# Performance work log

Hardware: AMD Instinct MI355X
Metric: run time of the kernel (lower is better)

Reference implementation:

```python
import jax, jax.numpy as jnp
import numpy as np

N = 384        # n_res
C = 128        # c_pair
H = 4          # num_head
DH = C // H    # qkv_dim = 32
LN_EPS = 1e-5
NEG_INF = -1e9


def setup_inputs() -> dict:
    key = jax.random.key(0)
    ks = jax.random.split(key, 8)
    s = 0.02
    return {
        "pair": jax.random.normal(ks[0], (N, N, C), dtype=jnp.float32),
        "mask": jax.random.randint(ks[1], (N, N), 0, 2, dtype=jnp.int32),
        "ln_w": jnp.ones((C,), dtype=jnp.float32),
        "ln_b": jnp.zeros((C,), dtype=jnp.float32),
        "w_bias": jax.random.normal(ks[2], (C, H), dtype=jnp.float32) * s,
        "wq": jax.random.normal(ks[3], (C, C), dtype=jnp.float32) * s,
        "wk": jax.random.normal(ks[4], (C, C), dtype=jnp.float32) * s,
        "wv": jax.random.normal(ks[5], (C, C), dtype=jnp.float32) * s,
        "wg": jax.random.normal(ks[6], (C, C), dtype=jnp.float32) * s,
        "wo": jax.random.normal(ks[7], (C, C), dtype=jnp.float32) * s,
    }


def reference(pair, mask, ln_w, ln_b, w_bias, wq, wk, wv, wg, wo):
    # LayerNorm over c_pair (biased variance, as torch)
    mu = pair.mean(-1, keepdims=True)
    var = jnp.mean(jnp.square(pair - mu), axis=-1, keepdims=True)
    x = (pair - mu) * jax.lax.rsqrt(var + LN_EPS) * ln_w + ln_b  # [N,N,C]

    # per-head pair bias: [H, N, N] (query axis q, key axis k)
    bias = jnp.einsum('qkc,ch->hqk', x, w_bias)

    # QKV + gating projections (no bias)
    q = jnp.einsum('bkc,cd->bkd', x, wq).reshape(N, N, H, DH)
    k = jnp.einsum('bkc,cd->bkd', x, wk).reshape(N, N, H, DH)
    v = jnp.einsum('bkc,cd->bkd', x, wv).reshape(N, N, H, DH)

    scale = 1.0 / np.sqrt(DH).astype(np.float32)
    logits = jnp.einsum('bqhd,bkhd->bhqk', q, k) * scale + bias[None]  # [N,H,N,N]
    # mask[b, k]: disallow attending to masked keys in row b
    logits = jnp.where(mask[:, None, None, :] > 0, logits, NEG_INF)
    probs = jax.nn.softmax(logits, axis=-1)

    o = jnp.einsum('bhqk,bkhd->bqhd', probs, v).reshape(N, N, C)
    gate = jax.nn.sigmoid(jnp.einsum('bqc,cd->bqd', x, wg))
    out = jnp.einsum('bqc,cd->bqd', o * gate, wo)  # [N,N,C]
    return out
```

## Files before the change

kernel.cpp:

```cpp
#include <hip/hip_runtime.h>
#include <hip/hip_bf16.h>
#include <stdint.h>

#define NRES 384
#define CPAIR 128
#define NHEAD 4
#define DHEAD 32
#define MROWS (NRES * NRES)
#define QK_SCALE 0.17677669529663687f
#define LOG2E 1.4426950408889634f
#define QK_L2E (0.17677669529663687f * 1.4426950408889634f)

typedef unsigned short u16;
typedef short bf16x8 __attribute__((ext_vector_type(8)));
typedef float f32x4 __attribute__((ext_vector_type(4)));

__device__ __forceinline__ u16 f2bf(float f) {
  union { float f; uint32_t u; } c; c.f = f;
  uint32_t u = c.u + 0x7fff + ((c.u >> 16) & 1);
  return (u16)(u >> 16);
}
__device__ __forceinline__ float bf2f(u16 h) {
  union { uint32_t u; float f; } c; c.u = ((uint32_t)h) << 16; return c.f;
}
__device__ __forceinline__ float fast_exp2(float x) {
#if __has_builtin(__builtin_amdgcn_exp2f)
  return __builtin_amdgcn_exp2f(x);
#else
  return exp2f(x);
#endif
}
__device__ __forceinline__ uint32_t cvt_pk_bf16(float lo, float hi) {
  uint32_t r;
  asm("v_cvt_pk_bf16_f32 %0, %1, %2" : "=v"(r) : "v"(lo), "v"(hi));
  return r;
}

__global__ void prep_kernel(const float* __restrict__ wq, const float* __restrict__ wk,
                            const float* __restrict__ wv, const float* __restrict__ wg,
                            const float* __restrict__ wb, const float* __restrict__ wo,
                            u16* __restrict__ wcat, u16* __restrict__ wot) {
  int tid = blockIdx.x * blockDim.x + threadIdx.x;
  int stride = gridDim.x * blockDim.x;
  for (int i = tid; i < 576 * 128; i += stride) {
    int n = i >> 7, kk = i & 127;
    float val;
    if (n < 128)      val = wq[kk * 128 + n] * QK_L2E;
    else if (n < 256) val = wk[kk * 128 + (n - 128)];
    else if (n < 384) val = wv[kk * 128 + (n - 256)];
    else if (n < 512) val = wg[kk * 128 + (n - 384)];
    else if (n < 516) val = wb[kk * 4 + (n - 512)] * LOG2E;
    else              val = 0.f;
    wcat[i] = f2bf(val);
  }
  for (int i = tid; i < 128 * 128; i += stride) {
    int n = i >> 7, kk = i & 127;
    wot[i] = f2bf(wo[kk * 128 + n]);
  }
}

__global__ __launch_bounds__(256) void proj_kernel(
    const float* __restrict__ pair, const float* __restrict__ lnw,
    const float* __restrict__ lnb, const u16* __restrict__ wcat,
    u16* __restrict__ q, u16* __restrict__ k, u16* __restrict__ v,
    u16* __restrict__ g, float* __restrict__ biasL) {
  __shared__ __align__(16) u16 xs[64 * 136];
  __shared__ __align__(16) u16 wsm[64 * 136];
  const int m0 = blockIdx.x * 64;
  const int tid = threadIdx.x;
  {
    const int row = tid >> 2, q4 = tid & 3;
    const float* pr = pair + (size_t)(m0 + row) * CPAIR + q4 * 32;
    float4 vals[8];
    float s1 = 0.f, s2 = 0.f;
#pragma unroll
    for (int i = 0; i < 8; ++i) {
      vals[i] = ((const float4*)pr)[i];
      s1 += (vals[i].x + vals[i].y) + (vals[i].z + vals[i].w);
      s2 += vals[i].x * vals[i].x + vals[i].y * vals[i].y +
            vals[i].z * vals[i].z + vals[i].w * vals[i].w;
    }
    s1 += __shfl_xor(s1, 1); s1 += __shfl_xor(s1, 2);
    s2 += __shfl_xor(s2, 1); s2 += __shfl_xor(s2, 2);
    const float mu = s1 * (1.f / 128.f);
    const float rs = rsqrtf(s2 * (1.f / 128.f) - mu * mu + 1e-5f);
    const float* wr = lnw + q4 * 32;
    const float* br = lnb + q4 * 32;
    uint32_t packed[16];
#pragma unroll
    for (int i = 0; i < 8; ++i) {
      float4 w4 = ((const float4*)wr)[i];
      float4 b4 = ((const float4*)br)[i];
      float y0 = (vals[i].x - mu) * rs * w4.x + b4.x;
      float y1 = (vals[i].y - mu) * rs * w4.y + b4.y;
      float y2 = (vals[i].z - mu) * rs * w4.z + b4.z;
      float y3 = (vals[i].w - mu) * rs * w4.w + b4.w;
      packed[i * 2]     = (uint32_t)f2bf(y0) | ((uint32_t)f2bf(y1) << 16);
      packed[i * 2 + 1] = (uint32_t)f2bf(y2) | ((uint32_t)f2bf(y3) << 16);
    }
#pragma unroll
    for (int i = 0; i < 4; ++i)
      *(uint4*)&xs[row * 136 + q4 * 32 + i * 8] = *(uint4*)&packed[i * 4];
  }
  const int w = tid >> 6, lane = tid & 63, lm = lane & 15, quad = lane >> 4;
  for (int nc = 0; nc < 9; ++nc) {
    __syncthreads();
#pragma unroll
    for (int i = 0; i < 4; ++i) {
      int c = tid + i * 256;
      int row = c >> 4, col8 = (c & 15) * 8;
      *(uint4*)&wsm[row * 136 + col8] =
          *(const uint4*)&wcat[(size_t)(nc * 64 + row) * CPAIR + col8];
    }
    __syncthreads();
    f32x4 acc[4] = {{0, 0, 0, 0}, {0, 0, 0, 0}, {0, 0, 0, 0}, {0, 0, 0, 0}};
#pragma unroll
    for (int ks = 0; ks < 4; ++ks) {
      bf16x8 a = *(const bf16x8*)&xs[(w * 16 + lm) * 136 + ks * 32 + quad * 8];
#pragma unroll
      for (int nt = 0; nt < 4; ++nt) {
        bf16x8 bb = *(const bf16x8*)&wsm[(nt * 16 + lm) * 136 + ks * 32 + quad * 8];
        acc[nt] = __builtin_amdgcn_mfma_f32_16x16x32_bf16(a, bb, acc[nt], 0, 0, 0);
      }
    }
#pragma unroll
    for (int nt = 0; nt < 4; ++nt) {
      int n = nc * 64 + nt * 16 + lm;
#pragma unroll
      for (int r = 0; r < 4; ++r) {
        size_t m = (size_t)(m0 + w * 16 + quad * 4 + r);
        float val = acc[nt][r];
        if (n < 128)      q[m * CPAIR + n] = f2bf(val);
        else if (n < 256) k[m * CPAIR + (n - 128)] = f2bf(val);
        else if (n < 384) v[m * CPAIR + (n - 256)] = f2bf(val);
        else if (n < 512) g[m * CPAIR + (n - 384)] = f2bf(1.f / (1.f + __expf(-val)));
        else if (n < 516) {
          int h = n - 512;
          int q_idx = (int)(m / NRES), k_idx = (int)(m % NRES);
          int qt = q_idx >> 6, l6 = q_idx & 63;
          int ww = l6 >> 4, lmq = l6 & 15;
          int t = k_idx >> 4, qk = (k_idx >> 2) & 3, rk = k_idx & 3;
          size_t idx = ((size_t)((h * 6 + qt) * 24 + t) * 256 +
                        (ww * 64 + qk * 16 + lmq)) * 4 + rk;
          biasL[idx] = val;
        }
      }
    }
  }
}

__global__ __launch_bounds__(512, 4) void attn_kernel(
    const u16* __restrict__ q, const u16* __restrict__ k, const u16* __restrict__ v,
    const u16* __restrict__ g, const float* __restrict__ biasL, const int* __restrict__ mask,
    u16* __restrict__ og) {
  __shared__ __align__(16) u16 Ks[NRES * 40];
  __shared__ __align__(16) u16 Vt[DHEAD * 392];
  __shared__ __align__(16) float msk[NRES];

  const int b = blockIdx.x, h = blockIdx.y;
  const int tid = threadIdx.x;
  const int w = tid >> 6, lane = tid & 63, lm = lane & 15, quad = lane >> 4;
  const int wv = w & 3, hi = w >> 2;

  const u16* kb = k + (size_t)(b * NRES) * CPAIR + h * DHEAD;
  const u16* vb = v + (size_t)(b * NRES) * CPAIR + h * DHEAD;
  for (int i = tid; i < NRES * 4; i += 512) {
    int kk = i >> 2, c8 = (i & 3) * 8;
    *(uint4*)&Ks[kk * 40 + c8] = *(const uint4*)&kb[(size_t)kk * CPAIR + c8];
  }
  for (int i = tid; i < NRES * 4; i += 512) {
    int d8 = i & 3, kk = i >> 2;
    bf16x8 val = *(const bf16x8*)&vb[(size_t)kk * CPAIR + d8 * 8];
    int G = (kk >> 5) * 4 + ((kk >> 2) & 3);
    int e = (kk & 3) + 4 * ((kk >> 4) & 1);
    int col = (((G ^ d8) << 3) | e);
#pragma unroll
    for (int j = 0; j < 8; ++j) Vt[(d8 * 8 + j) * 392 + col] = (u16)val[j];
  }
  for (int i = tid; i < NRES; i += 512)
    msk[i] = (mask[b * NRES + i] > 0) ? 1.f : 0.f;
  __syncthreads();

  const int f0 = lm >> 3, f1 = (lm + 16) >> 3;

  for (int it = 0; it < 3; ++it) {
    const int qt = hi * 3 + it;
    const int q0 = qt * 64;
    bf16x8 af = *(const bf16x8*)&q[(size_t)(b * NRES + q0 + wv * 16 + lm) * CPAIR +
                                   h * DHEAD + quad * 8];
    const float* bptr = biasL + ((size_t)(h * 6 + qt) * 24) * 1024 + (wv * 64 + lane) * 4;
    float rsum = 0.f;
    f32x4 o0 = {0, 0, 0, 0}, o1 = {0, 0, 0, 0};
#pragma unroll
    for (int c = 0; c < 12; ++c) {
      f32x4 s[2];
#pragma unroll
      for (int tl = 0; tl < 2; ++tl) {
        int t = c * 2 + tl;
        bf16x8 kf = *(const bf16x8*)&Ks[(t * 16 + lm) * 40 + quad * 8];
        f32x4 bv = *(const f32x4*)(bptr + t * 1024);
        s[tl] = __builtin_amdgcn_mfma_f32_16x16x32_bf16(kf, af, bv, 0, 0, 0);
      }
      uint32_t pw[4];
#pragma unroll
      for (int tl = 0; tl < 2; ++tl) {
        int t = c * 2 + tl;
        f32x4 m4 = *(const f32x4*)&msk[t * 16 + quad * 4];
        float p0 = fast_exp2(s[tl][0]) * m4[0];
        float p1 = fast_exp2(s[tl][1]) * m4[1];
        float p2 = fast_exp2(s[tl][2]) * m4[2];
        float p3 = fast_exp2(s[tl][3]) * m4[3];
        rsum += (p0 + p1) + (p2 + p3);
        pw[tl * 2]     = cvt_pk_bf16(p0, p1);
        pw[tl * 2 + 1] = cvt_pk_bf16(p2, p3);
      }
      union { uint32_t u[4]; bf16x8 v8; } pf;
      pf.u[0] = pw[0]; pf.u[1] = pw[1]; pf.u[2] = pw[2]; pf.u[3] = pw[3];
      int B0i = c * 4 + quad;
      bf16x8 vt0 = *(const bf16x8*)&Vt[lm * 392 + ((B0i ^ f0) << 3)];
      bf16x8 vt1 = *(const bf16x8*)&Vt[(lm + 16) * 392 + ((B0i ^ f1) << 3)];
      o0 = __builtin_amdgcn_mfma_f32_16x16x32_bf16(pf.v8, vt0, o0, 0, 0, 0);
      o1 = __builtin_amdgcn_mfma_f32_16x16x32_bf16(pf.v8, vt1, o1, 0, 0, 0);
    }
    rsum += __shfl_xor(rsum, 16);
    rsum += __shfl_xor(rsum, 32);
#pragma unroll
    for (int r = 0; r < 4; ++r) {
      float rall = __shfl(rsum, quad * 4 + r);
      float rinv = 1.f / rall;
      size_t mrow = (size_t)(b * NRES + q0 + wv * 16 + quad * 4 + r);
      int c0 = h * DHEAD + lm, c1 = h * DHEAD + 16 + lm;
      float g0 = bf2f(g[mrow * CPAIR + c0]);
      float g1 = bf2f(g[mrow * CPAIR + c1]);
      og[mrow * CPAIR + c0] = f2bf(o0[r] * rinv * g0);
      og[mrow * CPAIR + c1] = f2bf(o1[r] * rinv * g1);
    }
  }
}

__global__ __launch_bounds__(256) void outproj_kernel(const u16* __restrict__ og,
                                                      const u16* __restrict__ wot,
                                                      float* __restrict__ out) {
  __shared__ __align__(16) u16 xs[64 * 136];
  __shared__ __align__(16) u16 wsm[64 * 136];
  const int m0 = blockIdx.x * 64;
  const int tid = threadIdx.x;
#pragma unroll
  for (int i = 0; i < 4; ++i) {
    int c = tid + i * 256;
    int row = c >> 4, col8 = (c & 15) * 8;
    *(uint4*)&xs[row * 136 + col8] = *(const uint4*)&og[(size_t)(m0 + row) * CPAIR + col8];
  }
  const int w = tid >> 6, lane = tid & 63, lm = lane & 15, quad = lane >> 4;
  for (int nc = 0; nc < 2; ++nc) {
    __syncthreads();
#pragma unroll
    for (int i = 0; i < 4; ++i) {
      int c = tid + i * 256;
      int row = c >> 4, col8 = (c & 15) * 8;
      *(uint4*)&wsm[row * 136 + col8] =
          *(const uint4*)&wot[(size_t)(nc * 64 + row) * CPAIR + col8];
    }
    __syncthreads();
    f32x4 acc[4] = {{0, 0, 0, 0}, {0, 0, 0, 0}, {0, 0, 0, 0}, {0, 0, 0, 0}};
#pragma unroll
    for (int ks = 0; ks < 4; ++ks) {
      bf16x8 a = *(const bf16x8*)&xs[(w * 16 + lm) * 136 + ks * 32 + quad * 8];
#pragma unroll
      for (int nt = 0; nt < 4; ++nt) {
        bf16x8 bb = *(const bf16x8*)&wsm[(nt * 16 + lm) * 136 + ks * 32 + quad * 8];
        acc[nt] = __builtin_amdgcn_mfma_f32_16x16x32_bf16(a, bb, acc[nt], 0, 0, 0);
      }
    }
#pragma unroll
    for (int nt = 0; nt < 4; ++nt) {
      int n = nc * 64 + nt * 16 + lm;
#pragma unroll
      for (int r = 0; r < 4; ++r) {
        size_t m = (size_t)(m0 + w * 16 + quad * 4 + r);
        out[m * CPAIR + n] = acc[nt][r];
      }
    }
  }
}

extern "C" void kernel_launch(void* const* d_in, const int* in_sizes, int n_in,
                              void* d_out, int out_size, void* d_ws, size_t ws_size,
                              hipStream_t stream) {
  const float* pair = (const float*)d_in[0];
  const int* mask = (const int*)d_in[1];
  const float* ln_w = (const float*)d_in[2];
  const float* ln_b = (const float*)d_in[3];
  const float* w_bias = (const float*)d_in[4];
  const float* wq = (const float*)d_in[5];
  const float* wk = (const float*)d_in[6];
  const float* wv = (const float*)d_in[7];
  const float* wg = (const float*)d_in[8];
  const float* wo = (const float*)d_in[9];
  float* out = (float*)d_out;

  u16* qb = (u16*)d_out;
  u16* gb = qb + (size_t)MROWS * CPAIR;

  char* ws = (char*)d_ws;
  const size_t SZ = (size_t)MROWS * CPAIR * 2;
  u16* og = (u16*)(ws);
  u16* kb = (u16*)(ws + SZ);
  u16* vb = (u16*)(ws + 2 * SZ);
  float* biasL = (float*)(ws + 3 * SZ);
  u16* wcat = (u16*)(ws + 3 * SZ + (size_t)NHEAD * MROWS * 4);
  u16* wot = wcat + 576 * 128;

  hipLaunchKernelGGL(prep_kernel, dim3(64), dim3(256), 0, stream,
                     wq, wk, wv, wg, w_bias, wo, wcat, wot);
  hipLaunchKernelGGL(proj_kernel, dim3(MROWS / 64), dim3(256), 0, stream,
                     pair, ln_w, ln_b, wcat, qb, kb, vb, gb, biasL);
  hipLaunchKernelGGL(attn_kernel, dim3(NRES, NHEAD), dim3(512), 0, stream,
                     qb, kb, vb, gb, biasL, mask, og);
  hipLaunchKernelGGL(outproj_kernel, dim3(MROWS / 64), dim3(256), 0, stream,
                     og, wot, out);
}
```

Baseline: 306.4 us.

## Hold A fragments in registers and read weights directly from global in projections

The projection kernel now handles 128 rows per block, with each wave holding two 16-row tiles. The LayerNorm'd activations are preloaded once into registers as MFMA A-fragments, and the weight tile is no longer staged through shared memory. Each weight fragment is read from global/L2 and reused across both row tiles. The output projection likewise loads its A fragments straight from global and reads weights directly, dropping its shared-memory staging and barriers. This removes per-chunk syncthreads and LDS round-trips, at the cost of more register pressure and uncoalesced-looking global weight reads that depend on cache hits.

```diff
diff --git a/kernel.cpp b/kernel.cpp
--- a/kernel.cpp
+++ b/kernel.cpp
@@ -64,12 +64,12 @@
     const float* __restrict__ lnb, const u16* __restrict__ wcat,
     u16* __restrict__ q, u16* __restrict__ k, u16* __restrict__ v,
     u16* __restrict__ g, float* __restrict__ biasL) {
-  __shared__ __align__(16) u16 xs[64 * 136];
-  __shared__ __align__(16) u16 wsm[64 * 136];
-  const int m0 = blockIdx.x * 64;
+  __shared__ __align__(16) u16 xs[128 * 136];
+  const int m0 = blockIdx.x * 128;
   const int tid = threadIdx.x;
-  {
-    const int row = tid >> 2, q4 = tid & 3;
+#pragma unroll
+  for (int half = 0; half < 2; ++half) {
+    const int row = (tid >> 2) + half * 64, q4 = tid & 3;
     const float* pr = pair + (size_t)(m0 + row) * CPAIR + q4 * 32;
     float4 vals[8];
     float s1 = 0.f, s2 = 0.f;
@@ -102,47 +102,52 @@
     for (int i = 0; i < 4; ++i)
       *(uint4*)&xs[row * 136 + q4 * 32 + i * 8] = *(uint4*)&packed[i * 4];
   }
+  __syncthreads();
+
   const int w = tid >> 6, lane = tid & 63, lm = lane & 15, quad = lane >> 4;
+  bf16x8 a[2][4];
+#pragma unroll
+  for (int mt = 0; mt < 2; ++mt)
+#pragma unroll
+    for (int ks = 0; ks < 4; ++ks)
+      a[mt][ks] = *(const bf16x8*)&xs[(w * 32 + mt * 16 + lm) * 136 + ks * 32 + quad * 8];
+
   for (int nc = 0; nc < 9; ++nc) {
-    __syncthreads();
-#pragma unroll
-    for (int i = 0; i < 4; ++i) {
-      int c = tid + i * 256;
-      int row = c >> 4, col8 = (c & 15) * 8;
-      *(uint4*)&wsm[row * 136 + col8] =
-          *(const uint4*)&wcat[(size_t)(nc * 64 + row) * CPAIR + col8];
-    }
-    __syncthreads();
-    f32x4 acc[4] = {{0, 0, 0, 0}, {0, 0, 0, 0}, {0, 0, 0, 0}, {0, 0, 0, 0}};
+    f32x4 acc[2][4] = {{{0,0,0,0},{0,0,0,0},{0,0,0,0},{0,0,0,0}},
+                       {{0,0,0,0},{0,0,0,0},{0,0,0,0},{0,0,0,0}}};
 #pragma unroll
     for (int ks = 0; ks < 4; ++ks) {
-      bf16x8 a = *(const bf16x8*)&xs[(w * 16 + lm) * 136 + ks * 32 + quad * 8];
 #pragma unroll
       for (int nt = 0; nt < 4; ++nt) {
-        bf16x8 bb = *(const bf16x8*)&wsm[(nt * 16 + lm) * 136 + ks * 32 + quad * 8];
-        acc[nt] = __builtin_amdgcn_mfma_f32_16x16x32_bf16(a, bb, acc[nt], 0, 0, 0);
-      }
-    }
-#pragma unroll
-    for (int nt = 0; nt < 4; ++nt) {
-      int n = nc * 64 + nt * 16 + lm;
-#pragma unroll
-      for (int r = 0; r < 4; ++r) {
-        size_t m = (size_t)(m0 + w * 16 + quad * 4 + r);
-        float val = acc[nt][r];
-        if (n < 128)      q[m * CPAIR + n] = f2bf(val);
-        else if (n < 256) k[m * CPAIR + (n - 128)] = f2bf(val);
-        else if (n < 384) v[m * CPAIR + (n - 256)] = f2bf(val);
-        else if (n < 512) g[m * CPAIR + (n - 384)] = f2bf(1.f / (1.f + __expf(-val)));
-        else if (n < 516) {
-          int h = n - 512;
-          int q_idx = (int)(m / NRES), k_idx = (int)(m % NRES);
-          int qt = q_idx >> 6, l6 = q_idx & 63;
-          int ww = l6 >> 4, lmq = l6 & 15;
-          int t = k_idx >> 4, qk = (k_idx >> 2) & 3, rk = k_idx & 3;
-          size_t idx = ((size_t)((h * 6 + qt) * 24 + t) * 256 +
-                        (ww * 64 + qk * 16 + lmq)) * 4 + rk;
-          biasL[idx] = val;
+        bf16x8 bb = *(const bf16x8*)&wcat[(size_t)(nc * 64 + nt * 16 + lm) * CPAIR +
+                                          ks * 32 + quad * 8];
+        acc[0][nt] = __builtin_amdgcn_mfma_f32_16x16x32_bf16(a[0][ks], bb, acc[0][nt], 0, 0, 0);
+        acc[1][nt] = __builtin_amdgcn_mfma_f32_16x16x32_bf16(a[1][ks], bb, acc[1][nt], 0, 0, 0);
+      }
+    }
+#pragma unroll
+    for (int mt = 0; mt < 2; ++mt) {
+#pragma unroll
+      for (int nt = 0; nt < 4; ++nt) {
+        int n = nc * 64 + nt * 16 + lm;
+#pragma unroll
+        for (int r = 0; r < 4; ++r) {
+          size_t m = (size_t)(m0 + w * 32 + mt * 16 + quad * 4 + r);
+          float val = acc[mt][nt][r];
+          if (n < 128)      q[m * CPAIR + n] = f2bf(val);
+          else if (n < 256) k[m * CPAIR + (n - 128)] = f2bf(val);
+          else if (n < 384) v[m * CPAIR + (n - 256)] = f2bf(val);
+          else if (n < 512) g[m * CPAIR + (n - 384)] = f2bf(1.f / (1.f + __expf(-val)));
+          else if (n < 516) {
+            int h = n - 512;
+            int q_idx = (int)(m / NRES), k_idx = (int)(m % NRES);
+            int qt = q_idx >> 6, l6 = q_idx & 63;
+            int ww = l6 >> 4, lmq = l6 & 15;
+            int t = k_idx >> 4, qk = (k_idx >> 2) & 3, rk = k_idx & 3;
+            size_t idx = ((size_t)((h * 6 + qt) * 24 + t) * 256 +
+                          (ww * 64 + qk * 16 + lmq)) * 4 + rk;
+            biasL[idx] = val;
+          }
         }
       }
     }
@@ -241,35 +246,23 @@
 __global__ __launch_bounds__(256) void outproj_kernel(const u16* __restrict__ og,
                                                       const u16* __restrict__ wot,
                                                       float* __restrict__ out) {
-  __shared__ __align__(16) u16 xs[64 * 136];
-  __shared__ __align__(16) u16 wsm[64 * 136];
   const int m0 = blockIdx.x * 64;
   const int tid = threadIdx.x;
-#pragma unroll
-  for (int i = 0; i < 4; ++i) {
-    int c = tid + i * 256;
-    int row = c >> 4, col8 = (c & 15) * 8;
-    *(uint4*)&xs[row * 136 + col8] = *(const uint4*)&og[(size_t)(m0 + row) * CPAIR + col8];
-  }
   const int w = tid >> 6, lane = tid & 63, lm = lane & 15, quad = lane >> 4;
+  bf16x8 a[4];
+#pragma unroll
+  for (int ks = 0; ks < 4; ++ks)
+    a[ks] = *(const bf16x8*)&og[(size_t)(m0 + w * 16 + lm) * CPAIR + ks * 32 + quad * 8];
+#pragma unroll
   for (int nc = 0; nc < 2; ++nc) {
-    __syncthreads();
-#pragma unroll
-    for (int i = 0; i < 4; ++i) {
-      int c = tid + i * 256;
-      int row = c >> 4, col8 = (c & 15) * 8;
-      *(uint4*)&wsm[row * 136 + col8] =
-          *(const uint4*)&wot[(size_t)(nc * 64 + row) * CPAIR + col8];
-    }
-    __syncthreads();
     f32x4 acc[4] = {{0, 0, 0, 0}, {0, 0, 0, 0}, {0, 0, 0, 0}, {0, 0, 0, 0}};
 #pragma unroll
     for (int ks = 0; ks < 4; ++ks) {
-      bf16x8 a = *(const bf16x8*)&xs[(w * 16 + lm) * 136 + ks * 32 + quad * 8];
 #pragma unroll
       for (int nt = 0; nt < 4; ++nt) {
-        bf16x8 bb = *(const bf16x8*)&wsm[(nt * 16 + lm) * 136 + ks * 32 + quad * 8];
-        acc[nt] = __builtin_amdgcn_mfma_f32_16x16x32_bf16(a, bb, acc[nt], 0, 0, 0);
+        bf16x8 bb = *(const bf16x8*)&wot[(size_t)(nc * 64 + nt * 16 + lm) * CPAIR +
+                                         ks * 32 + quad * 8];
+        acc[nt] = __builtin_amdgcn_mfma_f32_16x16x32_bf16(a[ks], bb, acc[nt], 0, 0, 0);
       }
     }
 #pragma unroll
@@ -313,7 +306,7 @@
 
   hipLaunchKernelGGL(prep_kernel, dim3(64), dim3(256), 0, stream,
                      wq, wk, wv, wg, w_bias, wo, wcat, wot);
-  hipLaunchKernelGGL(proj_kernel, dim3(MROWS / 64), dim3(256), 0, stream,
+  hipLaunchKernelGGL(proj_kernel, dim3(MROWS / 128), dim3(256), 0, stream,
                      pair, ln_w, ln_b, wcat, qb, kb, vb, gb, biasL);
   hipLaunchKernelGGL(attn_kernel, dim3(NRES, NHEAD), dim3(512), 0, stream,
                      qb, kb, vb, gb, biasL, mask, og);
```

Measured after the change: 371.5 us. 21.3% more time.

## Fold mask into bias, prefetch bias and gate, add MFMA priority hints

Applied to the files above, without the earlier changes.

The mask becomes an additive -4096 offset folded into the bias accumulator, which removes the per-element multiply after exp2. Bias tiles are software-prefetched two chunks ahead with double buffering, and gate values are loaded before the main loop so their global latency overlaps compute. s_setprio is raised around MFMA pairs to favour matrix issue. The exchange is more live registers, plus the assumption that the additive mask drives exp2 to zero for masked keys.

```diff
diff --git a/kernel.cpp b/kernel.cpp
--- a/kernel.cpp
+++ b/kernel.cpp
@@ -155,7 +155,7 @@
     u16* __restrict__ og) {
   __shared__ __align__(16) u16 Ks[NRES * 40];
   __shared__ __align__(16) u16 Vt[DHEAD * 392];
-  __shared__ __align__(16) float msk[NRES];
+  __shared__ __align__(16) float mskb[NRES];
 
   const int b = blockIdx.x, h = blockIdx.y;
   const int tid = threadIdx.x;
@@ -178,7 +178,7 @@
     for (int j = 0; j < 8; ++j) Vt[(d8 * 8 + j) * 392 + col] = (u16)val[j];
   }
   for (int i = tid; i < NRES; i += 512)
-    msk[i] = (mask[b * NRES + i] > 0) ? 1.f : 0.f;
+    mskb[i] = (mask[b * NRES + i] > 0) ? 0.f : -4096.f;
   __syncthreads();
 
   const int f0 = lm >> 3, f1 = (lm + 16) >> 3;
@@ -189,38 +189,57 @@
     bf16x8 af = *(const bf16x8*)&q[(size_t)(b * NRES + q0 + wv * 16 + lm) * CPAIR +
                                    h * DHEAD + quad * 8];
     const float* bptr = biasL + ((size_t)(h * 6 + qt) * 24) * 1024 + (wv * 64 + lane) * 4;
+
+    float gv0[4], gv1[4];
+#pragma unroll
+    for (int r = 0; r < 4; ++r) {
+      size_t mrow = (size_t)(b * NRES + q0 + wv * 16 + quad * 4 + r);
+      gv0[r] = bf2f(g[mrow * CPAIR + h * DHEAD + lm]);
+      gv1[r] = bf2f(g[mrow * CPAIR + h * DHEAD + 16 + lm]);
+    }
+
+    f32x4 bvp[2][2];
+    bvp[0][0] = *(const f32x4*)(bptr + 0 * 1024);
+    bvp[0][1] = *(const f32x4*)(bptr + 1 * 1024);
+    bvp[1][0] = *(const f32x4*)(bptr + 2 * 1024);
+    bvp[1][1] = *(const f32x4*)(bptr + 3 * 1024);
+
     float rsum = 0.f;
     f32x4 o0 = {0, 0, 0, 0}, o1 = {0, 0, 0, 0};
 #pragma unroll
     for (int c = 0; c < 12; ++c) {
-      f32x4 s[2];
-#pragma unroll
-      for (int tl = 0; tl < 2; ++tl) {
-        int t = c * 2 + tl;
-        bf16x8 kf = *(const bf16x8*)&Ks[(t * 16 + lm) * 40 + quad * 8];
-        f32x4 bv = *(const f32x4*)(bptr + t * 1024);
-        s[tl] = __builtin_amdgcn_mfma_f32_16x16x32_bf16(kf, af, bv, 0, 0, 0);
-      }
-      uint32_t pw[4];
-#pragma unroll
-      for (int tl = 0; tl < 2; ++tl) {
-        int t = c * 2 + tl;
-        f32x4 m4 = *(const f32x4*)&msk[t * 16 + quad * 4];
-        float p0 = fast_exp2(s[tl][0]) * m4[0];
-        float p1 = fast_exp2(s[tl][1]) * m4[1];
-        float p2 = fast_exp2(s[tl][2]) * m4[2];
-        float p3 = fast_exp2(s[tl][3]) * m4[3];
-        rsum += (p0 + p1) + (p2 + p3);
-        pw[tl * 2]     = cvt_pk_bf16(p0, p1);
-        pw[tl * 2 + 1] = cvt_pk_bf16(p2, p3);
-      }
+      const int t0 = c * 2, t1 = c * 2 + 1;
+      f32x4 mq0 = *(const f32x4*)&mskb[t0 * 16 + quad * 4];
+      f32x4 mq1 = *(const f32x4*)&mskb[t1 * 16 + quad * 4];
+      f32x4 cv0 = bvp[c & 1][0] + mq0;
+      f32x4 cv1 = bvp[c & 1][1] + mq1;
+      if (c < 10) {
+        bvp[c & 1][0] = *(const f32x4*)(bptr + (t0 + 4) * 1024);
+        bvp[c & 1][1] = *(const f32x4*)(bptr + (t1 + 4) * 1024);
+      }
+      bf16x8 kf0 = *(const bf16x8*)&Ks[(t0 * 16 + lm) * 40 + quad * 8];
+      bf16x8 kf1 = *(const bf16x8*)&Ks[(t1 * 16 + lm) * 40 + quad * 8];
+      __builtin_amdgcn_s_setprio(1);
+      f32x4 s0 = __builtin_amdgcn_mfma_f32_16x16x32_bf16(kf0, af, cv0, 0, 0, 0);
+      f32x4 s1 = __builtin_amdgcn_mfma_f32_16x16x32_bf16(kf1, af, cv1, 0, 0, 0);
+      __builtin_amdgcn_s_setprio(0);
+      float p00 = fast_exp2(s0[0]), p01 = fast_exp2(s0[1]);
+      float p02 = fast_exp2(s0[2]), p03 = fast_exp2(s0[3]);
+      float p10 = fast_exp2(s1[0]), p11 = fast_exp2(s1[1]);
+      float p12 = fast_exp2(s1[2]), p13 = fast_exp2(s1[3]);
+      rsum += ((p00 + p01) + (p02 + p03)) + ((p10 + p11) + (p12 + p13));
       union { uint32_t u[4]; bf16x8 v8; } pf;
-      pf.u[0] = pw[0]; pf.u[1] = pw[1]; pf.u[2] = pw[2]; pf.u[3] = pw[3];
+      pf.u[0] = cvt_pk_bf16(p00, p01);
+      pf.u[1] = cvt_pk_bf16(p02, p03);
+      pf.u[2] = cvt_pk_bf16(p10, p11);
+      pf.u[3] = cvt_pk_bf16(p12, p13);
       int B0i = c * 4 + quad;
       bf16x8 vt0 = *(const bf16x8*)&Vt[lm * 392 + ((B0i ^ f0) << 3)];
       bf16x8 vt1 = *(const bf16x8*)&Vt[(lm + 16) * 392 + ((B0i ^ f1) << 3)];
+      __builtin_amdgcn_s_setprio(1);
       o0 = __builtin_amdgcn_mfma_f32_16x16x32_bf16(pf.v8, vt0, o0, 0, 0, 0);
       o1 = __builtin_amdgcn_mfma_f32_16x16x32_bf16(pf.v8, vt1, o1, 0, 0, 0);
+      __builtin_amdgcn_s_setprio(0);
     }
     rsum += __shfl_xor(rsum, 16);
     rsum += __shfl_xor(rsum, 32);
@@ -230,10 +249,8 @@
       float rinv = 1.f / rall;
       size_t mrow = (size_t)(b * NRES + q0 + wv * 16 + quad * 4 + r);
       int c0 = h * DHEAD + lm, c1 = h * DHEAD + 16 + lm;
-      float g0 = bf2f(g[mrow * CPAIR + c0]);
-      float g1 = bf2f(g[mrow * CPAIR + c1]);
-      og[mrow * CPAIR + c0] = f2bf(o0[r] * rinv * g0);
-      og[mrow * CPAIR + c1] = f2bf(o1[r] * rinv * g1);
+      og[mrow * CPAIR + c0] = f2bf(o0[r] * rinv * gv0[r]);
+      og[mrow * CPAIR + c1] = f2bf(o1[r] * rinv * gv1[r]);
     }
   }
 }
```

Result: faster. 285.1 us (-7.0%).
